# Optimization experiments

Hardware: AMD Instinct MI355X
Metric: run time of the kernel (lower is better)

## Reference

```python
import math
import jax, jax.numpy as jnp
import numpy as np

B, N, G, D = 8, 1000, 1000, 2
E, H = 128, 8           # embedding_dim, n_heads
DH = E // H             # head dim
KNN = 16                # n_decoding_neighbors (static: mask all zeros -> K=min(16,N))
TANH_CLIP = 10.0


def make_heads(x, n_heads):
    # (B, n, E) -> (B, n_heads, n, E//n_heads)
    b, n, e = x.shape
    return x.reshape(b, n, n_heads, e // n_heads).transpose(0, 2, 1, 3)


def setup_inputs() -> dict:
    key = jax.random.key(0)
    ks = jax.random.split(key, 12)
    s = 1.0 / math.sqrt(E)
    return {
        "last_node": jax.random.randint(ks[0], (B, G), 0, N),
        "coordinates": jax.random.uniform(ks[1], (B, N, D), dtype=jnp.float32),
        "embeddings": jax.random.normal(ks[2], (B, N, E), dtype=jnp.float32),
        "group_ninf_mask": jnp.zeros((B, G, N), dtype=jnp.float32),
        "Wq_graph": jax.random.normal(ks[3], (E, E), dtype=jnp.float32) * s,
        "Wq_first": jax.random.normal(ks[4], (E, E), dtype=jnp.float32) * s,
        "Wq_last": jax.random.normal(ks[5], (E, E), dtype=jnp.float32) * s,
        "Wk": jax.random.normal(ks[6], (E, E), dtype=jnp.float32) * s,
        "Wv": jax.random.normal(ks[7], (E, E), dtype=jnp.float32) * s,
        "W_comb": jax.random.normal(ks[8], (E, E), dtype=jnp.float32) * s,
        "b_comb": jax.random.normal(ks[9], (E,), dtype=jnp.float32) * s,
    }


def reference(last_node, coordinates, embeddings, group_ninf_mask,
              Wq_graph, Wq_first, Wq_last, Wk, Wv, W_comb, b_comb):
    # --- reset() precomputation ---
    graph_emb = embeddings.mean(axis=1, keepdims=True)          # (B,1,E)
    q_graph = make_heads(graph_emb @ Wq_graph.T, H)             # (B,H,1,DH)
    k_h = make_heads(embeddings @ Wk.T, H)                      # (B,H,N,DH)
    v_h = make_heads(embeddings @ Wv.T, H)                      # (B,H,N,DH)

    # --- gather last node embedding ---
    idx_e = jnp.broadcast_to(last_node[..., None], (B, G, E))
    last_emb = jnp.take_along_axis(embeddings, idx_e, axis=1)   # (B,G,E)
    q_first = make_heads(last_emb @ Wq_first.T, H)              # (B,H,G,DH)
    q_last = make_heads(last_emb @ Wq_last.T, H)
    glimpse_q = q_graph + q_first + q_last                      # (B,H,G,DH)

    # --- KNN neighbor mask (cdist + topk + scatter) ---
    idx_c = jnp.broadcast_to(last_node[..., None], (B, G, D))
    last_coord = jnp.take_along_axis(coordinates, idx_c, axis=1)  # (B,G,D)
    d2 = (jnp.sum(last_coord**2, -1)[:, :, None]
          + jnp.sum(coordinates**2, -1)[:, None, :]
          - 2.0 * jnp.einsum('bgd,bnd->bgn', last_coord, coordinates))
    dist = jnp.sqrt(jnp.maximum(d2, 0.0))                       # (B,G,N)
    dist = jnp.where(group_ninf_mask == -jnp.inf, jnp.inf, dist)
    _, knn_idx = jax.lax.top_k(-dist, KNN)                      # (B,G,K) smallest dists
    bi = jnp.arange(B)[:, None, None]
    gi = jnp.arange(G)[None, :, None]
    glimpse_mask = jnp.full((B, G, N), -jnp.inf, dtype=jnp.float32)
    glimpse_mask = glimpse_mask.at[bi, gi, knn_idx].set(0.0)

    # --- masked multi-head glimpse attention ---
    scores = jnp.einsum('bhgd,bhnd->bhgn', glimpse_q, k_h) / math.sqrt(DH)
    scores = scores + glimpse_mask[:, None, :, :]
    attn = jax.nn.softmax(scores, axis=-1)
    out = jnp.einsum('bhgn,bhnd->bhgd', attn, v_h)              # (B,H,G,DH)
    out = out.transpose(0, 2, 1, 3).reshape(B, G, E)
    final_q = out @ W_comb.T + b_comb                           # (B,G,E)

    # --- tanh-clipped scoring + softmax ---
    score = jnp.einsum('bge,bne->bgn', final_q, embeddings) / math.sqrt(E)
    score_masked = TANH_CLIP * jnp.tanh(score) + group_ninf_mask
    probs = jax.nn.softmax(score_masked, axis=2)                # (B,G,N)
    return probs
```

## Files before the change

kernel.cpp:

```cpp
#include <hip/hip_runtime.h>
#include <math.h>

#define BD 8
#define NN 1000
#define GG 1000
#define EE 128

typedef unsigned long long u64;
typedef __attribute__((ext_vector_type(8))) short short8;
typedef __attribute__((ext_vector_type(4))) float f32x4;

#define OFF_QG    0
#define OFF_K     1024
#define OFF_V     (OFF_K + 1024000)
#define OFF_QFL   (OFF_V + 1024000)
#define OFF_OUTG  (OFF_QFL + 1024000)
#define OFF_FQ    (OFF_OUTG + 1024000)
#define OFF_PART  (OFF_FQ + 1024000)
#define OFF_GPART (OFF_PART + 64000)

__global__ __launch_bounds__(256) void k_gq1(const float* __restrict__ emb,
                                             float* __restrict__ gpart) {
  __shared__ float ps[2][128];
  int b = blockIdx.x, blk = blockIdx.y;
  int t = threadIdx.x;
  int e = t & 127, p = t >> 7;
  const float* eb = emb + ((size_t)b * NN + blk * 40 + p * 20) * EE + e;
  float s = 0.f;
#pragma unroll 4
  for (int n = 0; n < 20; ++n) s += eb[(size_t)n * EE];
  ps[p][e] = s;
  __syncthreads();
  if (t < 128) gpart[(b * 25 + blk) * 128 + t] = ps[0][t] + ps[1][t];
}

__global__ __launch_bounds__(128) void k_gq2(const float* __restrict__ gpart,
                                             const float* __restrict__ Wqg,
                                             float* __restrict__ qg) {
  __shared__ float ge[128];
  int b = blockIdx.x, t = threadIdx.x;
  float s = 0.f;
#pragma unroll 5
  for (int j = 0; j < 25; ++j) s += gpart[(b * 25 + j) * 128 + t];
  ge[t] = s * (1.f / 1000.f);
  __syncthreads();
  const float* wr = Wqg + (size_t)t * EE;
  float acc = 0.f;
#pragma unroll 8
  for (int k = 0; k < 128; ++k) acc += ge[k] * wr[k];
  qg[b * EE + t] = acc;
}

__global__ __launch_bounds__(256) void k_proj(const float* __restrict__ emb,
                                              const float* __restrict__ Wk,
                                              const float* __restrict__ Wv,
                                              const float* __restrict__ Wqf,
                                              const float* __restrict__ Wql,
                                              float* __restrict__ Karr,
                                              float* __restrict__ Varr,
                                              float* __restrict__ QFL) {
  __shared__ float Als[16][68];
  __shared__ float Bls[16][68];
  int mt = blockIdx.x, nt = blockIdx.y;
  int t = threadIdx.x;
  int ty = t >> 4, tx = t & 15;
  int row4 = t >> 2, kq = t & 3;
  float acc[4][4] = {};
  for (int k0 = 0; k0 < 128; k0 += 16) {
    const float* ap = emb + (size_t)(mt * 64 + row4) * EE + k0 + kq * 4;
    float4 av = *(const float4*)ap;
    int j = nt * 64 + row4;
    float4 bv;
    if (j < 128) {
      bv = *(const float4*)(Wk + (size_t)j * EE + k0 + kq * 4);
    } else if (j < 256) {
      bv = *(const float4*)(Wv + (size_t)(j - 128) * EE + k0 + kq * 4);
    } else {
      float4 f = *(const float4*)(Wqf + (size_t)(j - 256) * EE + k0 + kq * 4);
      float4 l = *(const float4*)(Wql + (size_t)(j - 256) * EE + k0 + kq * 4);
      bv = make_float4(f.x + l.x, f.y + l.y, f.z + l.z, f.w + l.w);
    }
    Als[kq * 4 + 0][row4] = av.x; Als[kq * 4 + 1][row4] = av.y;
    Als[kq * 4 + 2][row4] = av.z; Als[kq * 4 + 3][row4] = av.w;
    Bls[kq * 4 + 0][row4] = bv.x; Bls[kq * 4 + 1][row4] = bv.y;
    Bls[kq * 4 + 2][row4] = bv.z; Bls[kq * 4 + 3][row4] = bv.w;
    __syncthreads();
#pragma unroll
    for (int k = 0; k < 16; ++k) {
      float a0 = Als[k][ty * 4 + 0], a1 = Als[k][ty * 4 + 1];
      float a2 = Als[k][ty * 4 + 2], a3 = Als[k][ty * 4 + 3];
      float b0 = Bls[k][tx * 4 + 0], b1 = Bls[k][tx * 4 + 1];
      float b2 = Bls[k][tx * 4 + 2], b3 = Bls[k][tx * 4 + 3];
      acc[0][0] += a0 * b0; acc[0][1] += a0 * b1; acc[0][2] += a0 * b2; acc[0][3] += a0 * b3;
      acc[1][0] += a1 * b0; acc[1][1] += a1 * b1; acc[1][2] += a1 * b2; acc[1][3] += a1 * b3;
      acc[2][0] += a2 * b0; acc[2][1] += a2 * b1; acc[2][2] += a2 * b2; acc[2][3] += a2 * b3;
      acc[3][0] += a3 * b0; acc[3][1] += a3 * b1; acc[3][2] += a3 * b2; acc[3][3] += a3 * b3;
    }
    __syncthreads();
  }
  float* outp; int cb;
  if (nt < 2)      { outp = Karr; cb = nt * 64; }
  else if (nt < 4) { outp = Varr; cb = (nt - 2) * 64; }
  else             { outp = QFL;  cb = (nt - 4) * 64; }
#pragma unroll
  for (int i = 0; i < 4; ++i) {
    int r = mt * 64 + ty * 4 + i;
    float4 v = make_float4(acc[i][0], acc[i][1], acc[i][2], acc[i][3]);
    *(float4*)(outp + (size_t)r * EE + cb + tx * 4) = v;
  }
}

template <int CTRL>
__device__ __forceinline__ unsigned dpp_minu(unsigned x) {
  unsigned o = (unsigned)__builtin_amdgcn_update_dpp(0, (int)x, CTRL, 0xf, 0xf, false);
  return o < x ? o : x;
}
__device__ __forceinline__ unsigned wave_min_u32(unsigned x) {
  x = dpp_minu<0x121>(x);
  x = dpp_minu<0x122>(x);
  x = dpp_minu<0x124>(x);
  x = dpp_minu<0x128>(x);
  unsigned o = (unsigned)__shfl_xor((int)x, 16); x = o < x ? o : x;
  o = (unsigned)__shfl_xor((int)x, 32); x = o < x ? o : x;
  return x;
}

__global__ __launch_bounds__(256) void k_glimpse(const int* __restrict__ last_node,
                                                 const float* __restrict__ coords,
                                                 const float* __restrict__ mask,
                                                 const float* __restrict__ qg,
                                                 const float* __restrict__ QFL,
                                                 const float* __restrict__ Karr,
                                                 const float* __restrict__ Varr,
                                                 float* __restrict__ outg) {
  __shared__ float pbuf[4][128];
  __shared__ int   nbuf[4][16];
  const float INF = __builtin_inff();
  int wv = threadIdx.x >> 6;
  int lane = threadIdx.x & 63;
  int wid = (blockIdx.x * blockDim.x + threadIdx.x) >> 6;
  int b = wid / GG, g = wid % GG;
  int last = last_node[b * GG + g];
  const float2* cb2 = (const float2*)(coords + (size_t)b * NN * 2);
  float2 lc = cb2[last];
  float lc2 = lc.x * lc.x + lc.y * lc.y;
  const float* mrow = mask + ((size_t)b * GG + g) * NN;
  unsigned d2u[16];
#pragma unroll
  for (int i = 0; i < 16; ++i) {
    int n = lane + (i << 6);
    unsigned k = 0xFFFFFFFFu;
    if (n < NN) {
      float2 c = cb2[n];
      float d2 = lc2 + (c.x * c.x + c.y * c.y) - 2.f * (lc.x * c.x + lc.y * c.y);
      d2 = fmaxf(d2, 0.f);
      k = __float_as_uint(d2);
      if (mrow[n] == -INF) k = 0x7F800000u;
    }
    d2u[i] = k;
  }
  int h = lane >> 3;
  int kk = lane & 7;
  int n0sel = 0, n1sel = 0;
  for (int s = 0; s < 16; ++s) {
    unsigned bv = d2u[0]; int bs = 0;
#pragma unroll
    for (int i = 1; i < 16; ++i) {
      bool better = d2u[i] < bv;
      bv = better ? d2u[i] : bv;
      bs = better ? i : bs;
    }
    unsigned wm = wave_min_u32(bv);
    u64 tied = __ballot(bv == wm);
    int wn;
    if (__popcll(tied) == 1) {
      int wl = (int)__builtin_ctzll(tied);
      int ws = __builtin_amdgcn_readlane(bs, wl);
      wn = wl + (ws << 6);
    } else {
      unsigned cn = (bv == wm) ? (unsigned)(lane + (bs << 6)) : 0x7FFFFFFFu;
      cn = wave_min_u32(cn);
      wn = (int)__builtin_amdgcn_readfirstlane((int)cn);
    }
    n0sel = (s == kk) ? wn : n0sel;
    n1sel = (s == kk + 8) ? wn : n1sel;
    int iw = wn >> 6;
    bool me = (lane == (wn & 63));
#pragma unroll
    for (int i = 0; i < 16; ++i)
      if (i == iw && me) d2u[i] = 0xFFFFFFFFu;
  }
  float qh[16];
  {
    const float4* qg4 = (const float4*)(qg + b * EE + h * 16);
    const float4* qf4 = (const float4*)(QFL + ((size_t)b * NN + last) * EE + h * 16);
#pragma unroll
    for (int u = 0; u < 4; ++u) {
      float4 a = qg4[u], c = qf4[u];
      qh[u * 4 + 0] = a.x + c.x; qh[u * 4 + 1] = a.y + c.y;
      qh[u * 4 + 2] = a.z + c.z; qh[u * 4 + 3] = a.w + c.w;
    }
  }
  const float* Kb = Karr + (size_t)b * NN * EE;
  float s0 = 0.f, s1 = 0.f;
  {
    const float4* k04 = (const float4*)(Kb + (size_t)n0sel * EE + h * 16);
    const float4* k14 = (const float4*)(Kb + (size_t)n1sel * EE + h * 16);
    float4 ka[4], kb[4];
#pragma unroll
    for (int u = 0; u < 4; ++u) { ka[u] = k04[u]; kb[u] = k14[u]; }
#pragma unroll
    for (int u = 0; u < 4; ++u) {
      s0 += qh[u * 4 + 0] * ka[u].x; s0 += qh[u * 4 + 1] * ka[u].y;
      s0 += qh[u * 4 + 2] * ka[u].z; s0 += qh[u * 4 + 3] * ka[u].w;
      s1 += qh[u * 4 + 0] * kb[u].x; s1 += qh[u * 4 + 1] * kb[u].y;
      s1 += qh[u * 4 + 2] * kb[u].z; s1 += qh[u * 4 + 3] * kb[u].w;
    }
  }
  s0 *= 0.25f; s1 *= 0.25f;
  float m = fmaxf(s0, s1);
#pragma unroll
  for (int off = 1; off < 8; off <<= 1) m = fmaxf(m, __shfl_xor(m, off));
  float e0 = __expf(s0 - m), e1 = __expf(s1 - m);
  float se = e0 + e1;
#pragma unroll
  for (int off = 1; off < 8; off <<= 1) se += __shfl_xor(se, off);
  float p0 = e0 / se, p1 = e1 / se;
  pbuf[wv][h * 16 + kk] = p0;
  pbuf[wv][h * 16 + kk + 8] = p1;
  if (h == 0) { nbuf[wv][kk] = n0sel; nbuf[wv][kk + 8] = n1sel; }
  const float* Vb = Varr + (size_t)b * NN * EE;
  float o0 = 0.f, o1 = 0.f;
#pragma unroll
  for (int c = 0; c < 2; ++c) {
    int nk[8]; float pk[8]; float2 vv[8];
#pragma unroll
    for (int j = 0; j < 8; ++j) { nk[j] = nbuf[wv][c * 8 + j]; pk[j] = pbuf[wv][h * 16 + c * 8 + j]; }
#pragma unroll
    for (int j = 0; j < 8; ++j)
      vv[j] = *(const float2*)(Vb + (size_t)nk[j] * EE + h * 16 + kk * 2);
#pragma unroll
    for (int j = 0; j < 8; ++j) { o0 += pk[j] * vv[j].x; o1 += pk[j] * vv[j].y; }
  }
  *(float2*)(outg + ((size_t)b * GG + g) * EE + h * 16 + kk * 2) = make_float2(o0, o1);
}

__global__ __launch_bounds__(256) void k_comb(const float* __restrict__ outg,
                                              const float* __restrict__ Wc,
                                              const float* __restrict__ bc,
                                              float* __restrict__ fq) {
  __shared__ float Als[16][68];
  __shared__ float Bls[16][68];
  int mt = blockIdx.x, nt = blockIdx.y;
  int t = threadIdx.x;
  int ty = t >> 4, tx = t & 15;
  int row4 = t >> 2, kq = t & 3;
  float acc[4][4] = {};
  for (int k0 = 0; k0 < 128; k0 += 16) {
    float4 av = *(const float4*)(outg + (size_t)(mt * 64 + row4) * EE + k0 + kq * 4);
    int j = nt * 64 + row4;
    float4 bv = *(const float4*)(Wc + (size_t)j * EE + k0 + kq * 4);
    Als[kq * 4 + 0][row4] = av.x; Als[kq * 4 + 1][row4] = av.y;
    Als[kq * 4 + 2][row4] = av.z; Als[kq * 4 + 3][row4] = av.w;
    Bls[kq * 4 + 0][row4] = bv.x; Bls[kq * 4 + 1][row4] = bv.y;
    Bls[kq * 4 + 2][row4] = bv.z; Bls[kq * 4 + 3][row4] = bv.w;
    __syncthreads();
#pragma unroll
    for (int k = 0; k < 16; ++k) {
      float a0 = Als[k][ty * 4 + 0], a1 = Als[k][ty * 4 + 1];
      float a2 = Als[k][ty * 4 + 2], a3 = Als[k][ty * 4 + 3];
      float b0 = Bls[k][tx * 4 + 0], b1 = Bls[k][tx * 4 + 1];
      float b2 = Bls[k][tx * 4 + 2], b3 = Bls[k][tx * 4 + 3];
      acc[0][0] += a0 * b0; acc[0][1] += a0 * b1; acc[0][2] += a0 * b2; acc[0][3] += a0 * b3;
      acc[1][0] += a1 * b0; acc[1][1] += a1 * b1; acc[1][2] += a1 * b2; acc[1][3] += a1 * b3;
      acc[2][0] += a2 * b0; acc[2][1] += a2 * b1; acc[2][2] += a2 * b2; acc[2][3] += a2 * b3;
      acc[3][0] += a3 * b0; acc[3][1] += a3 * b1; acc[3][2] += a3 * b2; acc[3][3] += a3 * b3;
    }
    __syncthreads();
  }
#pragma unroll
  for (int i = 0; i < 4; ++i) {
    int r = mt * 64 + ty * 4 + i;
    int c = nt * 64 + tx * 4;
    float4 v = make_float4(acc[i][0] + bc[c + 0], acc[i][1] + bc[c + 1],
                           acc[i][2] + bc[c + 2], acc[i][3] + bc[c + 3]);
    *(float4*)(fq + (size_t)r * EE + c) = v;
  }
}

__global__ __launch_bounds__(256) void k_cvt(const float* __restrict__ src,
                                             short* __restrict__ dst) {
  int t = blockIdx.x, b = blockIdx.y;
  int w = threadIdx.x >> 6, l = threadIdx.x & 63;
  int r = min(t * 16 + (l & 15), NN - 1);
  int k = w * 32 + (l >> 4) * 8;
  const float* sp = src + ((size_t)b * NN + r) * EE + k;
  float4 v0 = *(const float4*)sp;
  float4 v1 = *(const float4*)(sp + 4);
  float x[8] = {v0.x, v0.y, v0.z, v0.w, v1.x, v1.y, v1.z, v1.w};
  short8 hv, mv, lv;
#pragma unroll
  for (int j = 0; j < 8; ++j) {
    float xv = x[j];
    unsigned uh = __float_as_uint(xv) & 0xFFFF0000u;
    hv[j] = (short)(uh >> 16);
    float r1 = xv - __uint_as_float(uh);
    unsigned um = __float_as_uint(r1) & 0xFFFF0000u;
    mv[j] = (short)(um >> 16);
    float r2 = r1 - __uint_as_float(um);
    lv[j] = (short)(__float_as_uint(r2) >> 16);
  }
  short* dbase = dst + ((size_t)b * 393216 + (size_t)((t * 4 + w) * 3) * 512 + l * 8);
  *(short8*)(dbase)        = hv;
  *(short8*)(dbase + 512)  = mv;
  *(short8*)(dbase + 1024) = lv;
}

__global__ __launch_bounds__(256) void k_score(const short* __restrict__ fq3,
                                               const short* __restrict__ emb3,
                                               const float* __restrict__ mask,
                                               float* __restrict__ out,
                                               float* __restrict__ part) {
  int nt = blockIdx.x, gt = blockIdx.y, b = blockIdx.z;
  int w = threadIdx.x >> 6, l = threadIdx.x & 63;
  int gtile = gt * 4 + w;
  const short* ab = fq3 + ((size_t)b * 393216 + (size_t)gtile * 4 * 3 * 512 + l * 8);
  const short* bb = emb3 + ((size_t)b * 393216 + (size_t)nt * 8 * 4 * 3 * 512 + l * 8);
  f32x4 acc[8] = {};
#pragma unroll
  for (int k0 = 0; k0 < 4; ++k0) {
    short8 ah = *(const short8*)(ab + (k0 * 3 + 0) * 512);
    short8 am = *(const short8*)(ab + (k0 * 3 + 1) * 512);
    short8 al = *(const short8*)(ab + (k0 * 3 + 2) * 512);
#pragma unroll
    for (int c = 0; c < 8; ++c) {
      const short* bp = bb + (size_t)((c * 4 + k0) * 3) * 512;
      short8 bh = *(const short8*)(bp);
      short8 bm = *(const short8*)(bp + 512);
      short8 bl = *(const short8*)(bp + 1024);
      acc[c] = __builtin_amdgcn_mfma_f32_16x16x32_bf16(ah, bh, acc[c], 0, 0, 0);
      acc[c] = __builtin_amdgcn_mfma_f32_16x16x32_bf16(am, bh, acc[c], 0, 0, 0);
      acc[c] = __builtin_amdgcn_mfma_f32_16x16x32_bf16(ah, bm, acc[c], 0, 0, 0);
      acc[c] = __builtin_amdgcn_mfma_f32_16x16x32_bf16(am, bm, acc[c], 0, 0, 0);
      acc[c] = __builtin_amdgcn_mfma_f32_16x16x32_bf16(al, bh, acc[c], 0, 0, 0);
      acc[c] = __builtin_amdgcn_mfma_f32_16x16x32_bf16(ah, bl, acc[c], 0, 0, 0);
    }
  }
  const float rs = 0.08838834764831845f;
  const float NEGINF = -__builtin_inff();
  int q = l >> 4, cl = l & 15;
  int gb = gt * 64 + w * 16 + q * 4;
  size_t brow = (size_t)b * GG;
#pragma unroll
  for (int r = 0; r < 4; ++r) {
    int g = gb + r;
    bool gv = (g < GG);
    size_t row = (brow + (gv ? g : GG - 1)) * (size_t)NN;
    float rsum = 0.f;
    float ev[8];
#pragma unroll
    for (int c = 0; c < 8; ++c) {
      int n = nt * 128 + c * 16 + cl;
      float mvv = (gv && n < NN) ? mask[row + n] : NEGINF;
      float sc = acc[c][r] * rs;
      float u = __expf(2.f * sc);
      float th = 1.f - 2.f * __builtin_amdgcn_rcpf(u + 1.f);
      float e = __expf(10.f * th + mvv);
      ev[c] = e;
      rsum += e;
    }
    if (gv) {
#pragma unroll
      for (int c = 0; c < 8; ++c) {
        int n = nt * 128 + c * 16 + cl;
        if (n < NN) out[row + n] = ev[c];
      }
    }
#pragma unroll
    for (int off = 1; off < 16; off <<= 1) rsum += __shfl_xor(rsum, off);
    if (cl == 0 && gv) part[(brow + g) * 8 + nt] = rsum;
  }
}

__global__ __launch_bounds__(256) void k_norm(const float* __restrict__ part,
                                              float* __restrict__ out) {
  int row = blockIdx.x;
  __shared__ float ssum;
  int t = threadIdx.x;
  float v = (t < 8) ? part[(size_t)row * 8 + t] : 0.f;
#pragma unroll
  for (int off = 1; off < 8; off <<= 1) v += __shfl_xor(v, off);
  if (t == 0) ssum = v;
  __syncthreads();
  float inv = 1.f / ssum;
  if (t < 250) {
    float4* o = (float4*)(out + (size_t)row * NN);
    float4 x = o[t];
    x.x *= inv; x.y *= inv; x.z *= inv; x.w *= inv;
    o[t] = x;
  }
}

extern "C" void kernel_launch(void* const* d_in, const int* in_sizes, int n_in,
                              void* d_out, int out_size, void* d_ws, size_t ws_size,
                              hipStream_t stream) {
  const int*   last_node = (const int*)d_in[0];
  const float* coords    = (const float*)d_in[1];
  const float* emb       = (const float*)d_in[2];
  const float* mask      = (const float*)d_in[3];
  const float* Wqg       = (const float*)d_in[4];
  const float* Wqf       = (const float*)d_in[5];
  const float* Wql       = (const float*)d_in[6];
  const float* Wk        = (const float*)d_in[7];
  const float* Wv        = (const float*)d_in[8];
  const float* Wc        = (const float*)d_in[9];
  const float* bc        = (const float*)d_in[10];
  float* out = (float*)d_out;
  float* ws  = (float*)d_ws;

  float* qg    = ws + OFF_QG;
  float* Karr  = ws + OFF_K;
  float* Varr  = ws + OFF_V;
  float* QFL   = ws + OFF_QFL;
  float* outg  = ws + OFF_OUTG;
  float* fq    = ws + OFF_FQ;
  float* part  = ws + OFF_PART;
  float* gpart = ws + OFF_GPART;
  short* emb3  = (short*)(ws + OFF_K);
  short* fq3   = (short*)(ws + OFF_QFL);

  k_gq1<<<dim3(BD, 25), dim3(256), 0, stream>>>(emb, gpart);
  k_gq2<<<dim3(BD), dim3(128), 0, stream>>>(gpart, Wqg, qg);
  k_proj<<<dim3(125, 6), dim3(256), 0, stream>>>(emb, Wk, Wv, Wqf, Wql, Karr, Varr, QFL);
  k_glimpse<<<dim3(2000), dim3(256), 0, stream>>>(last_node, coords, mask, qg, QFL, Karr, Varr, outg);
  k_comb<<<dim3(125, 2), dim3(256), 0, stream>>>(outg, Wc, bc, fq);
  k_cvt<<<dim3(64, BD), dim3(256), 0, stream>>>(emb, emb3);
  k_cvt<<<dim3(64, BD), dim3(256), 0, stream>>>(fq, fq3);
  k_score<<<dim3(8, 16, 8), dim3(256), 0, stream>>>(fq3, emb3, mask, out, part);
  k_norm<<<dim3(8000), dim3(256), 0, stream>>>(part, out);
}
```

Baseline: 210.3 us.

## Fuse split-bf16 conversion into comb GEMM and coalesce score epilogue via LDS

```diff
diff --git a/kernel.cpp b/kernel.cpp
--- a/kernel.cpp
+++ b/kernel.cpp
@@ -248,43 +248,76 @@
 __global__ __launch_bounds__(256) void k_comb(const float* __restrict__ outg,
                                               const float* __restrict__ Wc,
                                               const float* __restrict__ bc,
-                                              float* __restrict__ fq) {
+                                              short* __restrict__ fq3) {
   __shared__ float Als[16][68];
-  __shared__ float Bls[16][68];
-  int mt = blockIdx.x, nt = blockIdx.y;
+  __shared__ float Bls[16][132];
+  int mt = blockIdx.x;
   int t = threadIdx.x;
   int ty = t >> 4, tx = t & 15;
-  int row4 = t >> 2, kq = t & 3;
-  float acc[4][4] = {};
+  int la = t >> 2, akq = t & 3;
+  int lb = t >> 1, bkq = t & 1;
+  const float* apos = outg + (size_t)(mt * 64 + la) * EE + akq * 4;
+  const float* bpos = Wc + (size_t)lb * EE + bkq * 8;
+  float acc[4][8] = {};
+  float4 pa  = *(const float4*)apos;
+  float4 pb0 = *(const float4*)bpos;
+  float4 pb1 = *(const float4*)(bpos + 4);
   for (int k0 = 0; k0 < 128; k0 += 16) {
-    float4 av = *(const float4*)(outg + (size_t)(mt * 64 + row4) * EE + k0 + kq * 4);
-    int j = nt * 64 + row4;
-    float4 bv = *(const float4*)(Wc + (size_t)j * EE + k0 + kq * 4);
-    Als[kq * 4 + 0][row4] = av.x; Als[kq * 4 + 1][row4] = av.y;
-    Als[kq * 4 + 2][row4] = av.z; Als[kq * 4 + 3][row4] = av.w;
-    Bls[kq * 4 + 0][row4] = bv.x; Bls[kq * 4 + 1][row4] = bv.y;
-    Bls[kq * 4 + 2][row4] = bv.z; Bls[kq * 4 + 3][row4] = bv.w;
     __syncthreads();
+    Als[akq * 4 + 0][la] = pa.x;  Als[akq * 4 + 1][la] = pa.y;
+    Als[akq * 4 + 2][la] = pa.z;  Als[akq * 4 + 3][la] = pa.w;
+    Bls[bkq * 8 + 0][lb] = pb0.x; Bls[bkq * 8 + 1][lb] = pb0.y;
+    Bls[bkq * 8 + 2][lb] = pb0.z; Bls[bkq * 8 + 3][lb] = pb0.w;
+    Bls[bkq * 8 + 4][lb] = pb1.x; Bls[bkq * 8 + 5][lb] = pb1.y;
+    Bls[bkq * 8 + 6][lb] = pb1.z; Bls[bkq * 8 + 7][lb] = pb1.w;
+    __syncthreads();
+    if (k0 < 112) {
+      pa  = *(const float4*)(apos + k0 + 16);
+      pb0 = *(const float4*)(bpos + k0 + 16);
+      pb1 = *(const float4*)(bpos + k0 + 20);
+    }
 #pragma unroll
     for (int k = 0; k < 16; ++k) {
-      float a0 = Als[k][ty * 4 + 0], a1 = Als[k][ty * 4 + 1];
-      float a2 = Als[k][ty * 4 + 2], a3 = Als[k][ty * 4 + 3];
-      float b0 = Bls[k][tx * 4 + 0], b1 = Bls[k][tx * 4 + 1];
-      float b2 = Bls[k][tx * 4 + 2], b3 = Bls[k][tx * 4 + 3];
-      acc[0][0] += a0 * b0; acc[0][1] += a0 * b1; acc[0][2] += a0 * b2; acc[0][3] += a0 * b3;
-      acc[1][0] += a1 * b0; acc[1][1] += a1 * b1; acc[1][2] += a1 * b2; acc[1][3] += a1 * b3;
-      acc[2][0] += a2 * b0; acc[2][1] += a2 * b1; acc[2][2] += a2 * b2; acc[2][3] += a2 * b3;
-      acc[3][0] += a3 * b0; acc[3][1] += a3 * b1; acc[3][2] += a3 * b2; acc[3][3] += a3 * b3;
-    }
-    __syncthreads();
-  }
+      float4 av  = *(const float4*)&Als[k][ty * 4];
+      float4 bv0 = *(const float4*)&Bls[k][tx * 8];
+      float4 bv1 = *(const float4*)&Bls[k][tx * 8 + 4];
+      float af[4] = {av.x, av.y, av.z, av.w};
+      float bf[8] = {bv0.x, bv0.y, bv0.z, bv0.w, bv1.x, bv1.y, bv1.z, bv1.w};
+#pragma unroll
+      for (int i = 0; i < 4; ++i)
+#pragma unroll
+        for (int j = 0; j < 8; ++j) acc[i][j] += af[i] * bf[j];
+    }
+  }
+  int c0 = tx * 8;
+  float4 b0 = *(const float4*)(bc + c0);
+  float4 b1 = *(const float4*)(bc + c0 + 4);
+  float bias[8] = {b0.x, b0.y, b0.z, b0.w, b1.x, b1.y, b1.z, b1.w};
+  int k0f = tx >> 2;
+  int lsub = tx & 3;
 #pragma unroll
   for (int i = 0; i < 4; ++i) {
     int r = mt * 64 + ty * 4 + i;
-    int c = nt * 64 + tx * 4;
-    float4 v = make_float4(acc[i][0] + bc[c + 0], acc[i][1] + bc[c + 1],
-                           acc[i][2] + bc[c + 2], acc[i][3] + bc[c + 3]);
-    *(float4*)(fq + (size_t)r * EE + c) = v;
+    int b = r / GG;
+    int g = r - b * GG;
+    short8 hv, mv, lv;
+#pragma unroll
+    for (int j = 0; j < 8; ++j) {
+      float xv = acc[i][j] + bias[j];
+      unsigned uh = __float_as_uint(xv) & 0xFFFF0000u;
+      hv[j] = (short)(uh >> 16);
+      float r1 = xv - __uint_as_float(uh);
+      unsigned um = __float_as_uint(r1) & 0xFFFF0000u;
+      mv[j] = (short)(um >> 16);
+      float r2 = r1 - __uint_as_float(um);
+      lv[j] = (short)(__float_as_uint(r2) >> 16);
+    }
+    int tile = g >> 4;
+    int lanefrag = (g & 15) + lsub * 16;
+    short* dbase = fq3 + ((size_t)b * 393216 + (size_t)((tile * 4 + k0f) * 3) * 512 + lanefrag * 8);
+    *(short8*)(dbase)        = hv;
+    *(short8*)(dbase + 512)  = mv;
+    *(short8*)(dbase + 1024) = lv;
   }
 }
 
@@ -316,16 +349,17 @@
   *(short8*)(dbase + 1024) = lv;
 }
 
-__global__ __launch_bounds__(256) void k_score(const short* __restrict__ fq3,
-                                               const short* __restrict__ emb3,
-                                               const float* __restrict__ mask,
-                                               float* __restrict__ out,
-                                               float* __restrict__ part) {
+__global__ __launch_bounds__(256, 2) void k_score(const short* __restrict__ fq3,
+                                                  const short* __restrict__ emb3,
+                                                  const float* __restrict__ mask,
+                                                  float* __restrict__ out,
+                                                  float* __restrict__ part) {
+  __shared__ float xs[4][16][132];
   int nt = blockIdx.x, gt = blockIdx.y, b = blockIdx.z;
   int w = threadIdx.x >> 6, l = threadIdx.x & 63;
   int gtile = gt * 4 + w;
-  const short* ab = fq3 + ((size_t)b * 393216 + (size_t)gtile * 4 * 3 * 512 + l * 8);
-  const short* bb = emb3 + ((size_t)b * 393216 + (size_t)nt * 8 * 4 * 3 * 512 + l * 8);
+  const short* ab = fq3 + ((size_t)b * 393216 + (size_t)gtile * 6144 + l * 8);
+  const short* bb = emb3 + ((size_t)b * 393216 + (size_t)nt * 8 * 6144 + l * 8);
   f32x4 acc[8] = {};
 #pragma unroll
   for (int k0 = 0; k0 < 4; ++k0) {
@@ -334,7 +368,7 @@
     short8 al = *(const short8*)(ab + (k0 * 3 + 2) * 512);
 #pragma unroll
     for (int c = 0; c < 8; ++c) {
-      const short* bp = bb + (size_t)((c * 4 + k0) * 3) * 512;
+      const short* bp = bb + (size_t)(c * 6144 + k0 * 1536);
       short8 bh = *(const short8*)(bp);
       short8 bm = *(const short8*)(bp + 512);
       short8 bl = *(const short8*)(bp + 1024);
@@ -346,39 +380,43 @@
       acc[c] = __builtin_amdgcn_mfma_f32_16x16x32_bf16(ah, bl, acc[c], 0, 0, 0);
     }
   }
+  int q = l >> 4, cl = l & 15;
+#pragma unroll
+  for (int c = 0; c < 8; ++c)
+#pragma unroll
+    for (int r = 0; r < 4; ++r)
+      xs[w][q * 4 + r][c * 16 + cl] = acc[c][r];
   const float rs = 0.08838834764831845f;
   const float NEGINF = -__builtin_inff();
-  int q = l >> 4, cl = l & 15;
-  int gb = gt * 64 + w * 16 + q * 4;
+  int half = l >> 5, ln = l & 31;
+  int n0 = nt * 128 + ln * 4;
+  bool nv = (n0 < NN);
   size_t brow = (size_t)b * GG;
 #pragma unroll
-  for (int r = 0; r < 4; ++r) {
-    int g = gb + r;
+  for (int it = 0; it < 8; ++it) {
+    int row = it * 2 + half;
+    int g = gt * 64 + w * 16 + row;
     bool gv = (g < GG);
-    size_t row = (brow + (gv ? g : GG - 1)) * (size_t)NN;
+    size_t roff = (brow + (gv ? g : GG - 1)) * (size_t)NN;
+    f32x4 v = *(const f32x4*)&xs[w][row][ln * 4];
+    float4 mvv;
+    if (gv && nv) mvv = *(const float4*)(mask + roff + n0);
+    else mvv = make_float4(NEGINF, NEGINF, NEGINF, NEGINF);
+    float mva[4] = {mvv.x, mvv.y, mvv.z, mvv.w};
+    float e[4];
     float rsum = 0.f;
-    float ev[8];
-#pragma unroll
-    for (int c = 0; c < 8; ++c) {
-      int n = nt * 128 + c * 16 + cl;
-      float mvv = (gv && n < NN) ? mask[row + n] : NEGINF;
-      float sc = acc[c][r] * rs;
+#pragma unroll
+    for (int j = 0; j < 4; ++j) {
+      float sc = v[j] * rs;
       float u = __expf(2.f * sc);
       float th = 1.f - 2.f * __builtin_amdgcn_rcpf(u + 1.f);
-      float e = __expf(10.f * th + mvv);
-      ev[c] = e;
-      rsum += e;
-    }
-    if (gv) {
-#pragma unroll
-      for (int c = 0; c < 8; ++c) {
-        int n = nt * 128 + c * 16 + cl;
-        if (n < NN) out[row + n] = ev[c];
-      }
-    }
-#pragma unroll
-    for (int off = 1; off < 16; off <<= 1) rsum += __shfl_xor(rsum, off);
-    if (cl == 0 && gv) part[(brow + g) * 8 + nt] = rsum;
+      e[j] = __expf(10.f * th + mva[j]);
+      rsum += e[j];
+    }
+    if (gv && nv) *(float4*)(out + roff + n0) = make_float4(e[0], e[1], e[2], e[3]);
+#pragma unroll
+    for (int off = 1; off < 32; off <<= 1) rsum += __shfl_xor(rsum, off);
+    if (ln == 0 && gv) part[(brow + g) * 8 + nt] = rsum;
   }
 }
 
@@ -423,19 +461,17 @@
   float* Varr  = ws + OFF_V;
   float* QFL   = ws + OFF_QFL;
   float* outg  = ws + OFF_OUTG;
-  float* fq    = ws + OFF_FQ;
   float* part  = ws + OFF_PART;
   float* gpart = ws + OFF_GPART;
   short* emb3  = (short*)(ws + OFF_K);
-  short* fq3   = (short*)(ws + OFF_QFL);
+  short* fq3   = (short*)(ws + OFF_FQ);
 
   k_gq1<<<dim3(BD, 25), dim3(256), 0, stream>>>(emb, gpart);
   k_gq2<<<dim3(BD), dim3(128), 0, stream>>>(gpart, Wqg, qg);
   k_proj<<<dim3(125, 6), dim3(256), 0, stream>>>(emb, Wk, Wv, Wqf, Wql, Karr, Varr, QFL);
   k_glimpse<<<dim3(2000), dim3(256), 0, stream>>>(last_node, coords, mask, qg, QFL, Karr, Varr, outg);
-  k_comb<<<dim3(125, 2), dim3(256), 0, stream>>>(outg, Wc, bc, fq);
+  k_comb<<<dim3(125), dim3(256), 0, stream>>>(outg, Wc, bc, fq3);
   k_cvt<<<dim3(64, BD), dim3(256), 0, stream>>>(emb, emb3);
-  k_cvt<<<dim3(64, BD), dim3(256), 0, stream>>>(fq, fq3);
   k_score<<<dim3(8, 16, 8), dim3(256), 0, stream>>>(fq3, emb3, mask, out, part);
   k_norm<<<dim3(8000), dim3(256), 0, stream>>>(part, out);
 }
```

Measured after the change: 207.3 us. No clear change (-1.4%).
